# Kernel tuning notes

Hardware: AMD Instinct MI355X
Metric: run time of the kernel (lower is better)

The kernel has to match this reference:

```python
import jax, jax.numpy as jnp
import numpy as np

NUM_NODES = 1_000_000
MEM_DIM = 128
MSG_DIM = 128
B = 262_144


def setup_inputs() -> dict:
    key = jax.random.key(0)
    k1, k2, k3, k4, k5, k6, k7 = jax.random.split(key, 7)
    s = 1.0 / np.sqrt(MEM_DIM)
    return {
        "memory": jax.random.normal(k1, (NUM_NODES, MEM_DIM), jnp.float32) * 0.1,
        "last_update": jnp.zeros((NUM_NODES,), jnp.float32),
        "messages": jax.random.normal(k2, (B, MSG_DIM), jnp.float32),
        "timestamps": jax.random.uniform(k3, (B,), jnp.float32),
        "W_ih": jax.random.uniform(k4, (3 * MEM_DIM, MSG_DIM), jnp.float32, -s, s),
        "W_hh": jax.random.uniform(k5, (3 * MEM_DIM, MEM_DIM), jnp.float32, -s, s),
        "b_ih": jax.random.uniform(k6, (3 * MEM_DIM,), jnp.float32, -s, s),
        "b_hh": jax.random.uniform(k7, (3 * MEM_DIM,), jnp.float32, -s, s),
        "node_ids": jax.random.randint(jax.random.fold_in(key, 99), (B,), 0, NUM_NODES, jnp.int64 if jax.config.jax_enable_x64 else jnp.int32),
    }


def gru_cell(x, h, W_ih, W_hh, b_ih, b_hh):
    # torch.nn.GRUCell math
    gi = x @ W_ih.T + b_ih  # [B, 3H]
    gh = h @ W_hh.T + b_hh  # [B, 3H]
    i_r, i_z, i_n = jnp.split(gi, 3, axis=-1)
    h_r, h_z, h_n = jnp.split(gh, 3, axis=-1)
    r = jax.nn.sigmoid(i_r + h_r)
    z = jax.nn.sigmoid(i_z + h_z)
    n = jnp.tanh(i_n + r * h_n)
    return (1.0 - z) * n + z * h


def reference(memory, last_update, messages, timestamps, W_ih, W_hh, b_ih, b_hh, node_ids):
    # gather node memory rows
    h = memory[node_ids]  # [B, MEM_DIM]
    h_new = gru_cell(messages, h, W_ih, W_hh, b_ih, b_hh)
    # scatter updated state and timestamps back into persistent buffers
    memory_new = memory.at[node_ids].set(h_new)
    last_update_new = last_update.at[node_ids].set(timestamps)
    return memory_new, last_update_new
```

## Files before the change

kernel.cpp:

```cpp
#include <hip/hip_runtime.h>
#include <hip/hip_bf16.h>
#include <stdint.h>

#define NN   1000000
#define DD   128
#define BT   262144
#define TR   64
#define RPB  512
#define NT   (RPB / TR)
#define GRUB (BT / RPB)
#define WINBIT (1 << 30)

typedef __attribute__((ext_vector_type(8))) short bf16x8;
typedef __attribute__((ext_vector_type(4))) float f32x4;

__device__ __forceinline__ uint32_t f2bf2(float lo, float hi) {
    __hip_bfloat162 b = __float22bfloat162_rn(make_float2(lo, hi));
    uint32_t u; __builtin_memcpy(&u, &b, 4); return u;
}
__device__ __forceinline__ bf16x8 cvt8(float4 a, float4 b) {
    union { bf16x8 v; uint32_t u[4]; } r;
    r.u[0] = f2bf2(a.x, a.y);
    r.u[1] = f2bf2(a.z, a.w);
    r.u[2] = f2bf2(b.x, b.y);
    r.u[3] = f2bf2(b.z, b.w);
    return r.v;
}
__device__ __forceinline__ float bf2f(unsigned short s) {
    union { uint32_t u; float f; } c; c.u = ((uint32_t)s) << 16;
    return c.f;
}
__device__ __forceinline__ float fastrcp(float x) {
    return __builtin_amdgcn_rcpf(x);
}
__device__ __forceinline__ float sigmoid_f(float x) {
    return fastrcp(1.0f + __expf(-x));
}
__device__ __forceinline__ float tanh_f(float x) {
    return fmaf(2.0f, fastrcp(1.0f + __expf(-2.0f * x)), -1.0f);
}

__global__ __launch_bounds__(256) void k_init(int4* __restrict__ winner) {
    int i = blockIdx.x * 256 + threadIdx.x;
    if (i < NN / 4) winner[i] = make_int4(-1, -1, -1, -1);
}

__global__ __launch_bounds__(256) void k_winner(const int* __restrict__ node_ids,
                                                int* __restrict__ winner) {
    int i = blockIdx.x * 256 + threadIdx.x;
    if (i < BT) atomicMax(&winner[node_ids[i]], i);
}

__global__ __launch_bounds__(256) void k_copy(const float4* __restrict__ mem_in,
                                              const float* __restrict__ lu_in,
                                              const float* __restrict__ ts,
                                              const int* __restrict__ winner,
                                              float4* __restrict__ mem_out,
                                              float* __restrict__ lu_out) {
    const long NV4 = (long)NN * 32;
    const long TOTAL = NV4 + NN;
    long stride = (long)gridDim.x * 256;
    for (long i = blockIdx.x * 256L + threadIdx.x; i < TOTAL; i += stride) {
        if (i < NV4) {
            int node = (int)(i >> 5);
            if (winner[node] < 0) mem_out[i] = mem_in[i];
        } else {
            int v = (int)(i - NV4);
            int w = winner[v];
            lu_out[v] = (w >= 0) ? ts[w] : lu_in[v];
        }
    }
}

__global__ __launch_bounds__(512, 2) void k_gru(const float* __restrict__ memory,
                                                const float* __restrict__ messages,
                                                const float* __restrict__ W_ih,
                                                const float* __restrict__ W_hh,
                                                const float* __restrict__ b_ih,
                                                const float* __restrict__ b_hh,
                                                const int* __restrict__ node_ids,
                                                const int* __restrict__ winner,
                                                float* __restrict__ out_mem) {
    __shared__ unsigned short x_lds[2][TR * DD];
    __shared__ unsigned short h_lds[2][TR * DD];
    __shared__ int s_nid[RPB];

    const int tid = threadIdx.x;
    const int rowBase = blockIdx.x * RPB;

    for (int i = tid; i < RPB; i += 512) {
        int brow = rowBase + i;
        int nid = node_ids[brow];
        s_nid[i] = nid | ((winner[nid] == brow) ? WINBIT : 0);
    }
    __syncthreads();

    const int lane  = tid & 63;
    const int wave  = tid >> 6;
    const int l15   = lane & 15;
    const int khalf = lane >> 4;
    const int jcol  = wave * 16 + l15;

    bf16x8 wf[6][4];
#pragma unroll
    for (int g = 0; g < 3; ++g) {
#pragma unroll
        for (int ks = 0; ks < 4; ++ks) {
            const float* p = W_ih + (size_t)(g * 128 + jcol) * DD + ks * 32 + khalf * 8;
            wf[g][ks] = cvt8(*(const float4*)p, *(const float4*)(p + 4));
            const float* q = W_hh + (size_t)(g * 128 + jcol) * DD + ks * 32 + khalf * 8;
            wf[3 + g][ks] = cvt8(*(const float4*)q, *(const float4*)(q + 4));
        }
    }
    const float br = b_ih[jcol] + b_hh[jcol];
    const float bz = b_ih[128 + jcol] + b_hh[128 + jcol];
    const float bin = b_ih[256 + jcol];
    const float bhn = b_hh[256 + jcol];

    const int sr  = tid >> 4;
    const int sc8 = (tid & 15) * 8;
    const int swz = (sc8 * 2) ^ ((sr & 7) << 4);
    const int offH0 = sr * 256 + swz;
    const int offH1 = (32 + sr) * 256 + swz;

#define GLOAD(X0, X1, H0, H1, t, half)                                          \
    {                                                                           \
        int r_ = (t) * TR + (half) * 32 + sr;                                   \
        const float* xp_ = messages + (size_t)(rowBase + r_) * DD + sc8;        \
        X0 = ((const float4*)xp_)[0]; X1 = ((const float4*)xp_)[1];             \
        const float* hp_ = memory + (size_t)(s_nid[r_] & (WINBIT - 1)) * DD + sc8; \
        H0 = ((const float4*)hp_)[0]; H1 = ((const float4*)hp_)[1];             \
    }

    float4 xA0, xA1, hA0, hA1, xB0, xB1, hB0, hB1;
    GLOAD(xA0, xA1, hA0, hA1, 0, 0);
    GLOAD(xB0, xB1, hB0, hB1, 0, 1);

#pragma unroll 1
    for (int t = 0; t < NT; ++t) {
        const int buf = t & 1;
        char* xb = (char*)(&x_lds[buf][0]);
        char* hb = (char*)(&h_lds[buf][0]);
        *(bf16x8*)(xb + offH0) = cvt8(xA0, xA1);
        *(bf16x8*)(hb + offH0) = cvt8(hA0, hA1);
        *(bf16x8*)(xb + offH1) = cvt8(xB0, xB1);
        *(bf16x8*)(hb + offH1) = cvt8(hB0, hB1);
        if (t + 1 < NT) {
            GLOAD(xA0, xA1, hA0, hA1, t + 1, 0);
            GLOAD(xB0, xB1, hB0, hB1, t + 1, 1);
        }
        asm volatile("s_waitcnt lgkmcnt(0)" ::: "memory");
        __builtin_amdgcn_sched_barrier(0);
        __builtin_amdgcn_s_barrier();
        __builtin_amdgcn_sched_barrier(0);

#pragma unroll
        for (int sub = 0; sub < 4; ++sub) {
            const int arow = sub * 16 + l15;
            const char* xr = (const char*)(&x_lds[buf][0]) + arow * 256;
            const char* hr = (const char*)(&h_lds[buf][0]) + arow * 256;
            const int aswz = (arow & 7) << 4;
            bf16x8 ax[4], ah[4];
#pragma unroll
            for (int ks = 0; ks < 4; ++ks) {
                const int cb = (ks * 64 + khalf * 16) ^ aswz;
                ax[ks] = *(const bf16x8*)(xr + cb);
                ah[ks] = *(const bf16x8*)(hr + cb);
            }
            f32x4 a_r  = {br,  br,  br,  br};
            f32x4 a_z  = {bz,  bz,  bz,  bz};
            f32x4 a_in = {bin, bin, bin, bin};
            f32x4 a_hn = {bhn, bhn, bhn, bhn};
#pragma unroll
            for (int ks = 0; ks < 4; ++ks) {
                a_r  = __builtin_amdgcn_mfma_f32_16x16x32_bf16(ax[ks], wf[0][ks], a_r,  0, 0, 0);
                a_r  = __builtin_amdgcn_mfma_f32_16x16x32_bf16(ah[ks], wf[3][ks], a_r,  0, 0, 0);
                a_z  = __builtin_amdgcn_mfma_f32_16x16x32_bf16(ax[ks], wf[1][ks], a_z,  0, 0, 0);
                a_z  = __builtin_amdgcn_mfma_f32_16x16x32_bf16(ah[ks], wf[4][ks], a_z,  0, 0, 0);
                a_in = __builtin_amdgcn_mfma_f32_16x16x32_bf16(ax[ks], wf[2][ks], a_in, 0, 0, 0);
                a_hn = __builtin_amdgcn_mfma_f32_16x16x32_bf16(ah[ks], wf[5][ks], a_hn, 0, 0, 0);
            }
#pragma unroll
            for (int q = 0; q < 4; ++q) {
                const int rl = sub * 16 + khalf * 4 + q;
                const int tr = t * TR + rl;
                float rg = sigmoid_f(a_r[q]);
                float zg = sigmoid_f(a_z[q]);
                float ng = tanh_f(a_in[q] + rg * a_hn[q]);
                unsigned short hu = *(const unsigned short*)(
                    (const char*)(&h_lds[buf][0]) + rl * 256 + ((jcol * 2) ^ ((rl & 7) << 4)));
                float h = bf2f(hu);
                float hnew = fmaf(zg, h - ng, ng);
                int v = s_nid[tr];
                if (v & WINBIT)
                    out_mem[(size_t)(v & (WINBIT - 1)) * DD + jcol] = hnew;
            }
        }
    }
#undef GLOAD
}

extern "C" void kernel_launch(void* const* d_in, const int* in_sizes, int n_in,
                              void* d_out, int out_size, void* d_ws, size_t ws_size,
                              hipStream_t stream) {
    const float* memory      = (const float*)d_in[0];
    const float* last_update = (const float*)d_in[1];
    const float* messages    = (const float*)d_in[2];
    const float* timestamps  = (const float*)d_in[3];
    const float* W_ih        = (const float*)d_in[4];
    const float* W_hh        = (const float*)d_in[5];
    const float* b_ih        = (const float*)d_in[6];
    const float* b_hh        = (const float*)d_in[7];
    const int*   node_ids    = (const int*)d_in[8];

    float* out_mem = (float*)d_out;
    float* out_lu  = out_mem + (size_t)NN * DD;

    int* winner = (int*)d_ws;

    k_init<<<(NN / 4 + 255) / 256, 256, 0, stream>>>((int4*)winner);
    k_winner<<<BT / 256, 256, 0, stream>>>(node_ids, winner);
    k_copy<<<4096, 256, 0, stream>>>((const float4*)memory, last_update, timestamps,
                                     winner, (float4*)out_mem, out_lu);
    k_gru<<<GRUB, 512, 0, stream>>>(memory, messages, W_ih, W_hh, b_ih, b_hh,
                                    node_ids, winner, out_mem);
}
```

Before: 282.9 us.

## Stage winner hidden rows as bf16 in copy pass and read them in GEMM

The copy kernel now reads every memory row and, for nodes that have a winner, writes a bf16 copy of the row into a dense workspace buffer indexed by the winning batch row. The GRU GEMM kernel then loads h from this compact bf16 buffer, using the winner index, instead of gathering fp32 rows randomly from memory. This halves the h bytes the GEMM reads and makes that access denser. The copy pass now reads all memory rows rather than only non-winner ones and adds a scattered bf16 write. Occupancy hint changes to one block per CU, and the original path is kept as a fallback when the workspace is too small.

Measured after the change: 311.6 us. +10.1%, slower.

```diff
diff --git a/kernel.cpp b/kernel.cpp
--- a/kernel.cpp
+++ b/kernel.cpp
@@ -10,6 +10,8 @@
 #define NT   (RPB / TR)
 #define GRUB (BT / RPB)
 #define WINBIT (1 << 30)
+#define HG_OFF ((size_t)4 << 20)
+#define WS_NEEDED (HG_OFF + (size_t)BT * DD * 2)
 
 typedef __attribute__((ext_vector_type(8))) short bf16x8;
 typedef __attribute__((ext_vector_type(4))) float f32x4;
@@ -49,6 +51,35 @@
                                                 int* __restrict__ winner) {
     int i = blockIdx.x * 256 + threadIdx.x;
     if (i < BT) atomicMax(&winner[node_ids[i]], i);
+}
+
+__global__ __launch_bounds__(256) void k_copy2(const float4* __restrict__ mem_in,
+                                               const float* __restrict__ lu_in,
+                                               const float* __restrict__ ts,
+                                               const int* __restrict__ winner,
+                                               float4* __restrict__ mem_out,
+                                               float* __restrict__ lu_out,
+                                               unsigned short* __restrict__ hg) {
+    const long NV4 = (long)NN * 32;
+    const long TOTAL = NV4 + NN;
+    long stride = (long)gridDim.x * 256;
+    for (long i = blockIdx.x * 256L + threadIdx.x; i < TOTAL; i += stride) {
+        if (i < NV4) {
+            int node = (int)(i >> 5);
+            int w = winner[node];
+            float4 v = mem_in[i];
+            if (w < 0) {
+                mem_out[i] = v;
+            } else {
+                uint2 u = make_uint2(f2bf2(v.x, v.y), f2bf2(v.z, v.w));
+                *(uint2*)(hg + (size_t)w * DD + (i & 31) * 4) = u;
+            }
+        } else {
+            int v = (int)(i - NV4);
+            int w = winner[v];
+            lu_out[v] = (w >= 0) ? ts[w] : lu_in[v];
+        }
+    }
 }
 
 __global__ __launch_bounds__(256) void k_copy(const float4* __restrict__ mem_in,
@@ -72,18 +103,19 @@
     }
 }
 
-__global__ __launch_bounds__(512, 2) void k_gru(const float* __restrict__ memory,
-                                                const float* __restrict__ messages,
-                                                const float* __restrict__ W_ih,
-                                                const float* __restrict__ W_hh,
-                                                const float* __restrict__ b_ih,
-                                                const float* __restrict__ b_hh,
-                                                const int* __restrict__ node_ids,
-                                                const int* __restrict__ winner,
-                                                float* __restrict__ out_mem) {
+__global__ __launch_bounds__(512, 1) void k_gemm(const unsigned short* __restrict__ hg,
+                                                 const float* __restrict__ messages,
+                                                 const float* __restrict__ W_ih,
+                                                 const float* __restrict__ W_hh,
+                                                 const float* __restrict__ b_ih,
+                                                 const float* __restrict__ b_hh,
+                                                 const int* __restrict__ node_ids,
+                                                 const int* __restrict__ winner,
+                                                 float* __restrict__ out_mem) {
     __shared__ unsigned short x_lds[2][TR * DD];
     __shared__ unsigned short h_lds[2][TR * DD];
     __shared__ int s_nid[RPB];
+    __shared__ int s_hsrc[RPB];
 
     const int tid = threadIdx.x;
     const int rowBase = blockIdx.x * RPB;
@@ -91,7 +123,9 @@
     for (int i = tid; i < RPB; i += 512) {
         int brow = rowBase + i;
         int nid = node_ids[brow];
-        s_nid[i] = nid | ((winner[nid] == brow) ? WINBIT : 0);
+        int w = winner[nid];
+        s_nid[i] = nid | ((w == brow) ? WINBIT : 0);
+        s_hsrc[i] = w;
     }
     __syncthreads();
 
@@ -112,8 +146,8 @@
             wf[3 + g][ks] = cvt8(*(const float4*)q, *(const float4*)(q + 4));
         }
     }
-    const float br = b_ih[jcol] + b_hh[jcol];
-    const float bz = b_ih[128 + jcol] + b_hh[128 + jcol];
+    const float br  = b_ih[jcol] + b_hh[jcol];
+    const float bz  = b_ih[128 + jcol] + b_hh[128 + jcol];
     const float bin = b_ih[256 + jcol];
     const float bhn = b_hh[256 + jcol];
 
@@ -123,18 +157,20 @@
     const int offH0 = sr * 256 + swz;
     const int offH1 = (32 + sr) * 256 + swz;
 
-#define GLOAD(X0, X1, H0, H1, t, half)                                          \
+#define GLOAD(t)                                                                \
     {                                                                           \
-        int r_ = (t) * TR + (half) * 32 + sr;                                   \
-        const float* xp_ = messages + (size_t)(rowBase + r_) * DD + sc8;        \
-        X0 = ((const float4*)xp_)[0]; X1 = ((const float4*)xp_)[1];             \
-        const float* hp_ = memory + (size_t)(s_nid[r_] & (WINBIT - 1)) * DD + sc8; \
-        H0 = ((const float4*)hp_)[0]; H1 = ((const float4*)hp_)[1];             \
-    }
-
-    float4 xA0, xA1, hA0, hA1, xB0, xB1, hB0, hB1;
-    GLOAD(xA0, xA1, hA0, hA1, 0, 0);
-    GLOAD(xB0, xB1, hB0, hB1, 0, 1);
+        int r_ = (t) * TR + sr;                                                 \
+        const float* xp0_ = messages + (size_t)(rowBase + r_) * DD + sc8;       \
+        const float* xp1_ = messages + (size_t)(rowBase + r_ + 32) * DD + sc8;  \
+        xA0 = ((const float4*)xp0_)[0]; xA1 = ((const float4*)xp0_)[1];         \
+        xB0 = ((const float4*)xp1_)[0]; xB1 = ((const float4*)xp1_)[1];         \
+        hA = *(const bf16x8*)(hg + (size_t)s_hsrc[r_] * DD + sc8);              \
+        hB = *(const bf16x8*)(hg + (size_t)s_hsrc[r_ + 32] * DD + sc8);         \
+    }
+
+    float4 xA0, xA1, xB0, xB1;
+    bf16x8 hA, hB;
+    GLOAD(0);
 
 #pragma unroll 1
     for (int t = 0; t < NT; ++t) {
@@ -142,13 +178,10 @@
         char* xb = (char*)(&x_lds[buf][0]);
         char* hb = (char*)(&h_lds[buf][0]);
         *(bf16x8*)(xb + offH0) = cvt8(xA0, xA1);
-        *(bf16x8*)(hb + offH0) = cvt8(hA0, hA1);
         *(bf16x8*)(xb + offH1) = cvt8(xB0, xB1);
-        *(bf16x8*)(hb + offH1) = cvt8(hB0, hB1);
-        if (t + 1 < NT) {
-            GLOAD(xA0, xA1, hA0, hA1, t + 1, 0);
-            GLOAD(xB0, xB1, hB0, hB1, t + 1, 1);
-        }
+        *(bf16x8*)(hb + offH0) = hA;
+        *(bf16x8*)(hb + offH1) = hB;
+        if (t + 1 < NT) GLOAD(t + 1);
         asm volatile("s_waitcnt lgkmcnt(0)" ::: "memory");
         __builtin_amdgcn_sched_barrier(0);
         __builtin_amdgcn_s_barrier();
@@ -200,6 +233,134 @@
 #undef GLOAD
 }
 
+__global__ __launch_bounds__(512, 1) void k_gru_fb(const float* __restrict__ memory,
+                                                   const float* __restrict__ messages,
+                                                   const float* __restrict__ W_ih,
+                                                   const float* __restrict__ W_hh,
+                                                   const float* __restrict__ b_ih,
+                                                   const float* __restrict__ b_hh,
+                                                   const int* __restrict__ node_ids,
+                                                   const int* __restrict__ winner,
+                                                   float* __restrict__ out_mem) {
+    __shared__ unsigned short x_lds[2][TR * DD];
+    __shared__ unsigned short h_lds[2][TR * DD];
+    __shared__ int s_nid[RPB];
+
+    const int tid = threadIdx.x;
+    const int rowBase = blockIdx.x * RPB;
+
+    for (int i = tid; i < RPB; i += 512) {
+        int brow = rowBase + i;
+        int nid = node_ids[brow];
+        s_nid[i] = nid | ((winner[nid] == brow) ? WINBIT : 0);
+    }
+    __syncthreads();
+
+    const int lane  = tid & 63;
+    const int wave  = tid >> 6;
+    const int l15   = lane & 15;
+    const int khalf = lane >> 4;
+    const int jcol  = wave * 16 + l15;
+
+    bf16x8 wf[6][4];
+#pragma unroll
+    for (int g = 0; g < 3; ++g) {
+#pragma unroll
+        for (int ks = 0; ks < 4; ++ks) {
+            const float* p = W_ih + (size_t)(g * 128 + jcol) * DD + ks * 32 + khalf * 8;
+            wf[g][ks] = cvt8(*(const float4*)p, *(const float4*)(p + 4));
+            const float* q = W_hh + (size_t)(g * 128 + jcol) * DD + ks * 32 + khalf * 8;
+            wf[3 + g][ks] = cvt8(*(const float4*)q, *(const float4*)(q + 4));
+        }
+    }
+    const float br  = b_ih[jcol] + b_hh[jcol];
+    const float bz  = b_ih[128 + jcol] + b_hh[128 + jcol];
+    const float bin = b_ih[256 + jcol];
+    const float bhn = b_hh[256 + jcol];
+
+    const int sr  = tid >> 4;
+    const int sc8 = (tid & 15) * 8;
+    const int swz = (sc8 * 2) ^ ((sr & 7) << 4);
+    const int offH0 = sr * 256 + swz;
+    const int offH1 = (32 + sr) * 256 + swz;
+
+#define GLOADF(t)                                                               \
+    {                                                                           \
+        int r_ = (t) * TR + sr;                                                 \
+        const float* xp0_ = messages + (size_t)(rowBase + r_) * DD + sc8;       \
+        const float* xp1_ = messages + (size_t)(rowBase + r_ + 32) * DD + sc8;  \
+        xA0 = ((const float4*)xp0_)[0]; xA1 = ((const float4*)xp0_)[1];         \
+        xB0 = ((const float4*)xp1_)[0]; xB1 = ((const float4*)xp1_)[1];         \
+        const float* hp0_ = memory + (size_t)(s_nid[r_] & (WINBIT - 1)) * DD + sc8; \
+        const float* hp1_ = memory + (size_t)(s_nid[r_ + 32] & (WINBIT - 1)) * DD + sc8; \
+        hA0 = ((const float4*)hp0_)[0]; hA1 = ((const float4*)hp0_)[1];         \
+        hB0 = ((const float4*)hp1_)[0]; hB1 = ((const float4*)hp1_)[1];         \
+    }
+
+    float4 xA0, xA1, xB0, xB1, hA0, hA1, hB0, hB1;
+    GLOADF(0);
+
+#pragma unroll 1
+    for (int t = 0; t < NT; ++t) {
+        const int buf = t & 1;
+        char* xb = (char*)(&x_lds[buf][0]);
+        char* hb = (char*)(&h_lds[buf][0]);
+        *(bf16x8*)(xb + offH0) = cvt8(xA0, xA1);
+        *(bf16x8*)(xb + offH1) = cvt8(xB0, xB1);
+        *(bf16x8*)(hb + offH0) = cvt8(hA0, hA1);
+        *(bf16x8*)(hb + offH1) = cvt8(hB0, hB1);
+        if (t + 1 < NT) GLOADF(t + 1);
+        asm volatile("s_waitcnt lgkmcnt(0)" ::: "memory");
+        __builtin_amdgcn_sched_barrier(0);
+        __builtin_amdgcn_s_barrier();
+        __builtin_amdgcn_sched_barrier(0);
+
+#pragma unroll
+        for (int sub = 0; sub < 4; ++sub) {
+            const int arow = sub * 16 + l15;
+            const char* xr = (const char*)(&x_lds[buf][0]) + arow * 256;
+            const char* hr = (const char*)(&h_lds[buf][0]) + arow * 256;
+            const int aswz = (arow & 7) << 4;
+            bf16x8 ax[4], ah[4];
+#pragma unroll
+            for (int ks = 0; ks < 4; ++ks) {
+                const int cb = (ks * 64 + khalf * 16) ^ aswz;
+                ax[ks] = *(const bf16x8*)(xr + cb);
+                ah[ks] = *(const bf16x8*)(hr + cb);
+            }
+            f32x4 a_r  = {br,  br,  br,  br};
+            f32x4 a_z  = {bz,  bz,  bz,  bz};
+            f32x4 a_in = {bin, bin, bin, bin};
+            f32x4 a_hn = {bhn, bhn, bhn, bhn};
+#pragma unroll
+            for (int ks = 0; ks < 4; ++ks) {
+                a_r  = __builtin_amdgcn_mfma_f32_16x16x32_bf16(ax[ks], wf[0][ks], a_r,  0, 0, 0);
+                a_r  = __builtin_amdgcn_mfma_f32_16x16x32_bf16(ah[ks], wf[3][ks], a_r,  0, 0, 0);
+                a_z  = __builtin_amdgcn_mfma_f32_16x16x32_bf16(ax[ks], wf[1][ks], a_z,  0, 0, 0);
+                a_z  = __builtin_amdgcn_mfma_f32_16x16x32_bf16(ah[ks], wf[4][ks], a_z,  0, 0, 0);
+                a_in = __builtin_amdgcn_mfma_f32_16x16x32_bf16(ax[ks], wf[2][ks], a_in, 0, 0, 0);
+                a_hn = __builtin_amdgcn_mfma_f32_16x16x32_bf16(ah[ks], wf[5][ks], a_hn, 0, 0, 0);
+            }
+#pragma unroll
+            for (int q = 0; q < 4; ++q) {
+                const int rl = sub * 16 + khalf * 4 + q;
+                const int tr = t * TR + rl;
+                float rg = sigmoid_f(a_r[q]);
+                float zg = sigmoid_f(a_z[q]);
+                float ng = tanh_f(a_in[q] + rg * a_hn[q]);
+                unsigned short hu = *(const unsigned short*)(
+                    (const char*)(&h_lds[buf][0]) + rl * 256 + ((jcol * 2) ^ ((rl & 7) << 4)));
+                float h = bf2f(hu);
+                float hnew = fmaf(zg, h - ng, ng);
+                int v = s_nid[tr];
+                if (v & WINBIT)
+                    out_mem[(size_t)(v & (WINBIT - 1)) * DD + jcol] = hnew;
+            }
+        }
+    }
+#undef GLOADF
+}
+
 extern "C" void kernel_launch(void* const* d_in, const int* in_sizes, int n_in,
                               void* d_out, int out_size, void* d_ws, size_t ws_size,
                               hipStream_t stream) {
@@ -217,11 +378,22 @@
     float* out_lu  = out_mem + (size_t)NN * DD;
 
     int* winner = (int*)d_ws;
+    unsigned short* hg = (unsigned short*)((char*)d_ws + HG_OFF);
 
     k_init<<<(NN / 4 + 255) / 256, 256, 0, stream>>>((int4*)winner);
     k_winner<<<BT / 256, 256, 0, stream>>>(node_ids, winner);
-    k_copy<<<4096, 256, 0, stream>>>((const float4*)memory, last_update, timestamps,
-                                     winner, (float4*)out_mem, out_lu);
-    k_gru<<<GRUB, 512, 0, stream>>>(memory, messages, W_ih, W_hh, b_ih, b_hh,
-                                    node_ids, winner, out_mem);
-}
+
+    if (ws_size >= WS_NEEDED) {
+        k_copy2<<<4096, 256, 0, stream>>>((const float4*)memory, last_update,
+                                          timestamps, winner, (float4*)out_mem,
+                                          out_lu, hg);
+        k_gemm<<<GRUB, 512, 0, stream>>>(hg, messages, W_ih, W_hh, b_ih, b_hh,
+                                         node_ids, winner, out_mem);
+    } else {
+        k_copy<<<4096, 256, 0, stream>>>((const float4*)memory, last_update,
+                                         timestamps, winner, (float4*)out_mem,
+                                         out_lu);
+        k_gru_fb<<<GRUB, 512, 0, stream>>>(memory, messages, W_ih, W_hh,
+                                           b_ih, b_hh, node_ids, winner, out_mem);
+    }
+}
```
